# Performance work log

Measured on AMD Instinct MI355X. Metric: run time of the kernel, lower is better.

## Reference

```python
import jax, jax.numpy as jnp
import numpy as np

B, N, K = 8, 1024, 16        # graphs, points per graph, kNN fan-in (loop=True includes self)
LATENT = 256
EPS = 1e-5                   # PyG BatchNorm eps


def _bn(x, g, b):
    # training-mode batch norm over all leading (node/edge) dims, per channel
    ax = tuple(range(x.ndim - 1))
    mu = jnp.mean(x, axis=ax, keepdims=True)
    var = jnp.var(x, axis=ax, keepdims=True)
    return g * (x - mu) * jax.lax.rsqrt(var + EPS) + b


def setup_inputs() -> dict:
    key = jax.random.key(0)
    ks = jax.random.split(key, 12)

    def lin(k, fi, fo):
        s = (6.0 / (fi + fo)) ** 0.5
        kw, kb = jax.random.split(k)
        W = jax.random.uniform(kw, (fi, fo), jnp.float32, -s, s)
        bb = jax.random.uniform(kb, (fo,), jnp.float32, -s, s)
        return W, bb

    pos = jax.random.normal(ks[0], (B * N, 3), jnp.float32)
    batch = jnp.repeat(jnp.arange(B, dtype=jnp.int32), N)

    c1_W1, c1_b1 = lin(ks[1], 6, 64)
    c1_W2, c1_b2 = lin(ks[2], 64, 64)
    c2_W1, c2_b1 = lin(ks[3], 67, 64)
    c2_W2, c2_b2 = lin(ks[4], 64, 128)
    c2_W3, c2_b3 = lin(ks[5], 128, 1024)
    lin_W, lin_b = lin(ks[6], 1024, LATENT)

    return {
        "pos": pos, "batch": batch,
        "c1_W1": c1_W1, "c1_b1": c1_b1,
        "c1_g1": jnp.ones((64,), jnp.float32), "c1_be1": jnp.zeros((64,), jnp.float32),
        "c1_W2": c1_W2, "c1_b2": c1_b2,
        "c2_W1": c2_W1, "c2_b1": c2_b1,
        "c2_g1": jnp.ones((64,), jnp.float32), "c2_be1": jnp.zeros((64,), jnp.float32),
        "c2_W2": c2_W2, "c2_b2": c2_b2,
        "c2_g2": jnp.ones((128,), jnp.float32), "c2_be2": jnp.zeros((128,), jnp.float32),
        "c2_W3": c2_W3, "c2_b3": c2_b3,
        "lin_W": lin_W, "lin_b": lin_b,
        "lin_g": jnp.ones((LATENT,), jnp.float32), "lin_be": jnp.zeros((LATENT,), jnp.float32),
    }


def reference(pos, batch,
              c1_W1, c1_b1, c1_g1, c1_be1, c1_W2, c1_b2,
              c2_W1, c2_b1, c2_g1, c2_be1, c2_W2, c2_b2,
              c2_g2, c2_be2, c2_W3, c2_b3,
              lin_W, lin_b, lin_g, lin_be):
    # ---- kNN graph (per-graph, loop=True: self is nearest) ----
    p3 = pos.reshape(B, N, 3)
    sq = jnp.sum(p3 * p3, axis=-1)                                   # [B,N]
    d = sq[:, :, None] + sq[:, None, :] - 2.0 * jnp.einsum('bnd,bmd->bnm', p3, p3)
    _, nbr = jax.lax.top_k(-d, K)                                    # [B,N,K] neighbor ids
    idx = (nbr + (jnp.arange(B) * N)[:, None, None]).reshape(B * N, K)

    # ---- PointNetConv 1: gather -> MLP([6,64,64]) -> max aggregate ----
    pj = pos[idx]                                                    # [P,K,3]
    rel = pj - pos[:, None, :]                                       # [P,K,3]
    feat = jnp.concatenate([pj, rel], axis=-1)                       # [P,K,6]
    h = jax.nn.relu(_bn(feat @ c1_W1 + c1_b1, c1_g1, c1_be1))
    x1 = jnp.max(h @ c1_W2 + c1_b2, axis=1)                          # [P,64]

    # ---- PointNetConv 2: MLP([67,64,128,1024]) -> max aggregate ----
    feat2 = jnp.concatenate([x1[idx], rel], axis=-1)                 # [P,K,67]
    h = jax.nn.relu(_bn(feat2 @ c2_W1 + c2_b1, c2_g1, c2_be1))
    h = jax.nn.relu(_bn(h @ c2_W2 + c2_b2, c2_g2, c2_be2))
    x2 = jnp.max(h @ c2_W3 + c2_b3, axis=1)                          # [P,1024]

    # ---- global max pool per graph + final MLP (plain_last=False) ----
    g = x2.reshape(B, N, -1).max(axis=1)                             # [B,1024]
    return jax.nn.relu(_bn(g @ lin_W + lin_b, lin_g, lin_be))        # [B,LATENT]
```

## Files before the change

kernel.cpp:

```cpp
#include <hip/hip_runtime.h>
#include <hip/hip_cooperative_groups.h>
#include <math.h>

#define NB   8
#define NPTS 1024
#define PTS  8192
#define KNN  16
#define PK   (PTS*KNN)

typedef __attribute__((ext_vector_type(8))) _Float16 f16x8;
typedef __attribute__((ext_vector_type(4))) float f32x4;

__device__ __forceinline__ unsigned short f2h(float f) {
  _Float16 h = (_Float16)f;
  union { _Float16 h; unsigned short u; } c; c.h = h;
  return c.u;
}
__device__ __forceinline__ float h2f(unsigned short u) {
  union { unsigned short u; _Float16 h; } c; c.u = u;
  return (float)c.h;
}
__device__ __forceinline__ int lanerank(unsigned long long m) {
  return __builtin_amdgcn_mbcnt_hi((unsigned)(m >> 32),
         __builtin_amdgcn_mbcnt_lo((unsigned)m, 0));
}

__global__ __launch_bounds__(256) void knn_conv1_kernel(const float* __restrict__ pos,
    const float* __restrict__ W1, const float* __restrict__ b1,
    int* __restrict__ idx, float* __restrict__ rel,
    unsigned short* __restrict__ z1h, float* __restrict__ mid1) {
  __shared__ float px[NPTS], py[NPTS], pz[NPTS];
  __shared__ float feat[4][KNN][6];
  __shared__ float ls[256], ls2[256];
  const int t = threadIdx.x;
  const int wv = t >> 6, lane = t & 63;
  const int b = blockIdx.x;
  const int graph = b >> 8;
  const int base = graph << 10;
  for (int j = t; j < NPTS; j += 256) {
    px[j] = pos[3*(base+j)];
    py[j] = pos[3*(base+j)+1];
    pz[j] = pos[3*(base+j)+2];
  }
  __syncthreads();

  const int il = ((b & 255) << 2) + wv;
  const int i  = base + il;
  const float pix = px[il], piy = py[il], piz = pz[il];
  const float sqi = pix*pix + piy*piy + piz*piz;

  unsigned key[16];
  #pragma unroll
  for (int q = 0; q < 16; ++q) {
    const int j = (q << 6) + lane;
    const float x = px[j], y = py[j], z = pz[j];
    const float sqj = x*x + y*y + z*z;
    const float dt  = pix*x + piy*y + piz*z;
    const float d   = sqi + sqj - 2.0f*dt;
    const unsigned db = __float_as_uint(d);
    key[q] = (db >> 31) ? ~db : (db | 0x80000000u);
  }

  unsigned V = 0;
  #pragma unroll 1
  for (int bb = 31; bb >= 0; --bb) {
    const unsigned test = V | (1u << bb);
    int cnt = 0;
    #pragma unroll
    for (int q = 0; q < 16; ++q)
      cnt += __popcll(__ballot(key[q] < test));
    if (cnt < 16) V = test;
  }

  int c = 0;
  #pragma unroll
  for (int q = 0; q < 16; ++q)
    c += __popcll(__ballot(key[q] < V));

  int p_lt = 0, p_eq = c;
  #pragma unroll 1
  for (int q = 0; q < 16; ++q) {
    const unsigned long long mlt = __ballot(key[q] < V);
    const unsigned long long meq = __ballot(key[q] == V);
    int slot = -1;
    if (key[q] < V) slot = p_lt + lanerank(mlt);
    else if (key[q] == V) {
      const int s = p_eq + lanerank(meq);
      if (s < 16) slot = s;
    }
    if (slot >= 0) {
      const int j = (q << 6) + lane;
      const int r = i*KNN + slot;
      const float rx = px[j] - pix, ry = py[j] - piy, rz = pz[j] - piz;
      idx[r] = base + j;
      rel[3*r] = rx; rel[3*r+1] = ry; rel[3*r+2] = rz;
      feat[wv][slot][0] = px[j]; feat[wv][slot][1] = py[j]; feat[wv][slot][2] = pz[j];
      feat[wv][slot][3] = rx;    feat[wv][slot][4] = ry;    feat[wv][slot][5] = rz;
    }
    p_lt += __popcll(mlt);
    p_eq += __popcll(meq);
  }

  float w[6];
  #pragma unroll
  for (int q = 0; q < 6; ++q) w[q] = W1[q*64 + lane];
  const float bbv = b1[lane];
  float s = 0.0f, s2 = 0.0f;
  #pragma unroll
  for (int k = 0; k < KNN; ++k) {
    float z = bbv;
    #pragma unroll
    for (int q = 0; q < 6; ++q) z += feat[wv][k][q]*w[q];
    z1h[(size_t)(i*KNN + k)*64 + lane] = f2h(z);
    s += z; s2 += z*z;
  }
  ls[t] = s; ls2[t] = s2;
  __syncthreads();
  if (t < 64) {
    float a  = ls[t] + ls[t+64] + ls[t+128] + ls[t+192];
    float a2 = ls2[t] + ls2[t+64] + ls2[t+128] + ls2[t+192];
    const int cp = (b & 7) * 128;
    atomicAdd(&mid1[cp + t], a);
    atomicAdd(&mid1[cp + 64 + t], a2);
  }
}

__global__ __launch_bounds__(256) void wprep_kernel(const float* __restrict__ W3,
    const float* __restrict__ W2, const float* __restrict__ W1c2,
    const float* __restrict__ W2c1,
    unsigned short* __restrict__ W3T, unsigned short* __restrict__ W2T,
    unsigned short* __restrict__ w1T, unsigned short* __restrict__ W2c1T,
    float* __restrict__ mids) {
  const int b = blockIdx.x, t = threadIdx.x;
  if (b < 128) {
    const int k = b;
    const int ks = k >> 5, qd = (k >> 3) & 3, e = k & 7;
    for (int n = t; n < 1024; n += 256) {
      const int nb = n >> 4, mc = n & 15;
      W3T[((nb*4 + ks) << 9) + qd*128 + mc*8 + e] = f2h(W3[(size_t)k*1024 + n]);
    }
  } else if (b < 132) {
    for (int id = (b-128)*2048 + t; id < (b-127)*2048; id += 256) {
      const int n = id >> 6, k = id & 63;
      W2T[n*64 + k] = f2h(W2[k*128 + n]);
    }
  } else if (b < 136) {
    for (int id = (b-132)*1024 + t; id < (b-131)*1024; id += 256) {
      const int n = id >> 6, k = id & 63;
      w1T[n*64 + k] = f2h(W1c2[k*64 + n]);
    }
  } else if (b < 140) {
    for (int id = (b-136)*1024 + t; id < (b-135)*1024; id += 256) {
      const int n = id >> 6, k = id & 63;
      W2c1T[n*64 + k] = f2h(W2c1[k*64 + n]);
    }
  } else {
    for (int i2 = t; i2 < 4096; i2 += 256) mids[i2] = 0.0f;
  }
}

__global__ __launch_bounds__(256) void conv1_l2max_mfma(
    const unsigned short* __restrict__ z1h, const float* __restrict__ mid1,
    const float* __restrict__ g1, const float* __restrict__ be1,
    const unsigned short* __restrict__ W2T, const float* __restrict__ b2,
    unsigned short* __restrict__ x1h) {
  __shared__ unsigned short As[128*64];
  __shared__ float scl[64], shl[64];
  const int r0 = blockIdx.x * 128;
  const int t = threadIdx.x;
  const int lane = t & 63, w = t >> 6;
  const int quad = lane >> 4, mcol = lane & 15;
  const float invR = 1.0f / (float)PK;

  if (t < 64) {
    float s = 0.0f, s2 = 0.0f;
    #pragma unroll
    for (int k = 0; k < 8; ++k) { s += mid1[k*128 + t]; s2 += mid1[k*128 + 64 + t]; }
    const float mu  = s * invR;
    const float var = s2 * invR - mu*mu;
    const float sc  = g1[t] * rsqrtf(var + 1e-5f);
    scl[t] = sc; shl[t] = be1[t] - mu*sc;
  }
  __syncthreads();

  {
    const int kb = t & 7, rr = t >> 3;
    float sc[8], sh[8];
    #pragma unroll
    for (int q = 0; q < 8; ++q) { sc[q] = scl[kb*8 + q]; sh[q] = shl[kb*8 + q]; }
    #pragma unroll
    for (int it = 0; it < 4; ++it) {
      const int r = rr + it*32;
      union { uint4 v; unsigned short s[8]; } in;
      in.v = *(const uint4*)(z1h + (size_t)(r0 + r)*64 + kb*8);
      union { unsigned short s[8]; uint4 v; } o;
      #pragma unroll
      for (int q = 0; q < 8; ++q)
        o.s[q] = f2h(fmaxf(h2f(in.s[q])*sc[q] + sh[q], 0.0f));
      *(uint4*)(As + r*64 + ((kb ^ (r & 7)) * 8)) = o.v;
    }
  }
  __syncthreads();

  const int wrow = (w >> 1) * 64;
  const int wncol = (w & 1) * 32;

  f32x4 acc[4][2];
  #pragma unroll
  for (int mi = 0; mi < 4; ++mi)
    #pragma unroll
    for (int ni = 0; ni < 2; ++ni)
      acc[mi][ni] = (f32x4){0.f, 0.f, 0.f, 0.f};

  #pragma unroll
  for (int ks = 0; ks < 2; ++ks) {
    f16x8 af[4], bfr[2];
    #pragma unroll
    for (int mi = 0; mi < 4; ++mi) {
      const int row = wrow + mi*16 + mcol;
      af[mi] = *(const f16x8*)(As + row*64 + (((ks*4 + quad) ^ (row & 7)) * 8));
    }
    #pragma unroll
    for (int ni = 0; ni < 2; ++ni) {
      const int nr = wncol + ni*16 + mcol;
      bfr[ni] = *(const f16x8*)(W2T + nr*64 + ks*32 + quad*8);
    }
    #pragma unroll
    for (int mi = 0; mi < 4; ++mi)
      #pragma unroll
      for (int ni = 0; ni < 2; ++ni)
        acc[mi][ni] = __builtin_amdgcn_mfma_f32_16x16x32_f16(af[mi], bfr[ni], acc[mi][ni], 0, 0, 0);
  }

  float bb[2];
  #pragma unroll
  for (int ni = 0; ni < 2; ++ni) bb[ni] = b2[wncol + ni*16 + mcol];
  #pragma unroll
  for (int mi = 0; mi < 4; ++mi) {
    const int p = blockIdx.x*8 + (w >> 1)*4 + mi;
    #pragma unroll
    for (int ni = 0; ni < 2; ++ni) {
      f32x4 a = acc[mi][ni];
      float m = fmaxf(fmaxf(a[0], a[1]), fmaxf(a[2], a[3]));
      m = fmaxf(m, __shfl_xor(m, 16));
      m = fmaxf(m, __shfl_xor(m, 32));
      if (quad == 0) x1h[(size_t)p*64 + wncol + ni*16 + mcol] = f2h(m + bb[ni]);
    }
  }
}

__global__ __launch_bounds__(256) void conv2_l1_mfma(
    const unsigned short* __restrict__ x1h, const int* __restrict__ idx,
    const float* __restrict__ rel, const unsigned short* __restrict__ w1T,
    const float* __restrict__ W1full, const float* __restrict__ b1,
    unsigned short* __restrict__ zah, float* __restrict__ midA) {
  __shared__ unsigned short S[128*64];
  __shared__ int   idxr[128];
  __shared__ float rl[128*3];
  __shared__ float ps[256];
  const int r0 = blockIdx.x * 128;
  const int t = threadIdx.x;
  const int lane = t & 63, w = t >> 6;
  const int quad = lane >> 4, mcol = lane & 15;

  if (t < 128) idxr[t] = idx[r0 + t];
  else if (t < 224) *(float4*)(rl + (t-128)*4) = *(const float4*)(rel + (size_t)r0*3 + (t-128)*4);
  __syncthreads();

  {
    const int kb = t & 7, rr = t >> 3;
    #pragma unroll
    for (int it = 0; it < 4; ++it) {
      const int r = rr + it*32;
      const int gj = idxr[r];
      const uint4 v = *(const uint4*)(x1h + (size_t)gj*64 + kb*8);
      *(uint4*)(S + r*64 + ((kb ^ (r & 7)) * 8)) = v;
    }
  }
  __syncthreads();

  const int wrow = (w >> 1) * 64;
  const int wcol = (w & 1) * 32;

  f16x8 af[2][4], bfr[2][2];
  #pragma unroll
  for (int ks = 0; ks < 2; ++ks)
    #pragma unroll
    for (int mi = 0; mi < 4; ++mi) {
      const int row = wrow + mi*16 + mcol;
      af[ks][mi] = *(const f16x8*)(S + row*64 + (((ks*4 + quad) ^ (row & 7)) * 8));
    }
  #pragma unroll
  for (int ks = 0; ks < 2; ++ks)
    #pragma unroll
    for (int ni = 0; ni < 2; ++ni) {
      const int nr = wcol + ni*16 + mcol;
      bfr[ks][ni] = *(const f16x8*)(w1T + nr*64 + ks*32 + quad*8);
    }

  f32x4 acc[4][2];
  #pragma unroll
  for (int mi = 0; mi < 4; ++mi)
    #pragma unroll
    for (int ni = 0; ni < 2; ++ni)
      acc[mi][ni] = (f32x4){0.f, 0.f, 0.f, 0.f};

  #pragma unroll
  for (int ks = 0; ks < 2; ++ks)
    #pragma unroll
    for (int mi = 0; mi < 4; ++mi)
      #pragma unroll
      for (int ni = 0; ni < 2; ++ni)
        acc[mi][ni] = __builtin_amdgcn_mfma_f32_16x16x32_f16(af[ks][mi], bfr[ks][ni], acc[mi][ni], 0, 0, 0);

  __syncthreads();

  float bb[2], wr0[2], wr1[2], wr2[2];
  #pragma unroll
  for (int ni = 0; ni < 2; ++ni) {
    const int col = wcol + ni*16 + mcol;
    bb[ni]  = b1[col];
    wr0[ni] = W1full[64*64 + col];
    wr1[ni] = W1full[65*64 + col];
    wr2[ni] = W1full[66*64 + col];
  }
  float s[2] = {0,0}, s2[2] = {0,0};
  #pragma unroll
  for (int mi = 0; mi < 4; ++mi) {
    #pragma unroll
    for (int j = 0; j < 4; ++j) {
      const int row = wrow + mi*16 + quad*4 + j;
      const float r0v = rl[row*3], r1v = rl[row*3+1], r2v = rl[row*3+2];
      #pragma unroll
      for (int ni = 0; ni < 2; ++ni) {
        const int col = wcol + ni*16 + mcol;
        const int g = col >> 3, o = col & 7;
        const float v = acc[mi][ni][j] + bb[ni] + r0v*wr0[ni] + r1v*wr1[ni] + r2v*wr2[ni];
        S[row*64 + ((g ^ (row & 7)) << 3) + o] = f2h(v);
        s[ni] += v; s2[ni] += v*v;
      }
    }
  }
  #pragma unroll
  for (int ni = 0; ni < 2; ++ni) {
    s[ni]  += __shfl_xor(s[ni], 16);  s[ni]  += __shfl_xor(s[ni], 32);
    s2[ni] += __shfl_xor(s2[ni], 16); s2[ni] += __shfl_xor(s2[ni], 32);
  }
  if (quad == 0) {
    const int rh = w >> 1;
    #pragma unroll
    for (int ni = 0; ni < 2; ++ni) {
      const int col = wcol + ni*16 + mcol;
      ps[rh*128 + col]      = s[ni];
      ps[rh*128 + 64 + col] = s2[ni];
    }
  }
  __syncthreads();

  #pragma unroll
  for (int i = 0; i < 4; ++i) {
    const int u = i*256 + t;
    const int row = u >> 3, gg = u & 7;
    *(uint4*)(zah + (size_t)(r0 + row)*64 + gg*8) =
        *(const uint4*)(S + row*64 + ((gg ^ (row & 7)) << 3));
  }
  if (t < 128) atomicAdd(&midA[(blockIdx.x & 7)*128 + t], ps[t] + ps[128 + t]);
}

__global__ __launch_bounds__(256) void conv2_l2_mfma(
    const unsigned short* __restrict__ zah, const float* __restrict__ midA,
    const float* __restrict__ g1, const float* __restrict__ be1,
    const unsigned short* __restrict__ W2T, const float* __restrict__ b2,
    unsigned short* __restrict__ zhb, float* __restrict__ midB) {
  __shared__ unsigned short S[128*128];
  __shared__ float ps[512];
  __shared__ float scl[64], shl[64];
  const int r0 = blockIdx.x * 128;
  const int t = threadIdx.x;
  const int lane = t & 63, w = t >> 6;
  const int quad = lane >> 4, mcol = lane & 15;
  const float invR = 1.0f / (float)PK;

  if (t < 64) {
    float s = 0.0f, s2 = 0.0f;
    #pragma unroll
    for (int k = 0; k < 8; ++k) { s += midA[k*128 + t]; s2 += midA[k*128 + 64 + t]; }
    const float mu  = s * invR;
    const float var = s2 * invR - mu*mu;
    const float sc  = g1[t] * rsqrtf(var + 1e-5f);
    scl[t] = sc; shl[t] = be1[t] - mu*sc;
  }
  __syncthreads();

  {
    const int kb = t & 7, rr = t >> 3;
    float sc[8], sh[8];
    #pragma unroll
    for (int q = 0; q < 8; ++q) { sc[q] = scl[kb*8 + q]; sh[q] = shl[kb*8 + q]; }
    #pragma unroll
    for (int it = 0; it < 4; ++it) {
      const int r = rr + it*32;
      union { uint4 v; unsigned short s[8]; } in;
      in.v = *(const uint4*)(zah + (size_t)(r0 + r)*64 + kb*8);
      union { unsigned short s[8]; uint4 v; } o;
      #pragma unroll
      for (int q = 0; q < 8; ++q)
        o.s[q] = f2h(fmaxf(h2f(in.s[q])*sc[q] + sh[q], 0.0f));
      *(uint4*)(S + r*64 + ((kb ^ (r & 7)) * 8)) = o.v;
    }
  }
  __syncthreads();

  const int wrow = (w >> 1) * 64;
  const int wcol = (w & 1) * 64;

  f16x8 af[2][4], bfr[2][4];
  #pragma unroll
  for (int ks = 0; ks < 2; ++ks)
    #pragma unroll
    for (int mi = 0; mi < 4; ++mi) {
      const int row = wrow + mi*16 + mcol;
      af[ks][mi] = *(const f16x8*)(S + row*64 + (((ks*4 + quad) ^ (row & 7)) * 8));
    }
  #pragma unroll
  for (int ks = 0; ks < 2; ++ks)
    #pragma unroll
    for (int ni = 0; ni < 4; ++ni) {
      const int nr = wcol + ni*16 + mcol;
      bfr[ks][ni] = *(const f16x8*)(W2T + nr*64 + ks*32 + quad*8);
    }

  f32x4 acc[4][4];
  #pragma unroll
  for (int mi = 0; mi < 4; ++mi)
    #pragma unroll
    for (int ni = 0; ni < 4; ++ni)
      acc[mi][ni] = (f32x4){0.f, 0.f, 0.f, 0.f};

  #pragma unroll
  for (int ks = 0; ks < 2; ++ks)
    #pragma unroll
    for (int mi = 0; mi < 4; ++mi)
      #pragma unroll
      for (int ni = 0; ni < 4; ++ni)
        acc[mi][ni] = __builtin_amdgcn_mfma_f32_16x16x32_f16(af[ks][mi], bfr[ks][ni], acc[mi][ni], 0, 0, 0);

  __syncthreads();

  float bb[4];
  #pragma unroll
  for (int ni = 0; ni < 4; ++ni) bb[ni] = b2[wcol + ni*16 + mcol];
  float s[4] = {0,0,0,0}, s2[4] = {0,0,0,0};
  #pragma unroll
  for (int mi = 0; mi < 4; ++mi) {
    #pragma unroll
    for (int ni = 0; ni < 4; ++ni) {
      const int col = wcol + ni*16 + mcol;
      const int g = col >> 3, o = col & 7;
      #pragma unroll
      for (int j = 0; j < 4; ++j) {
        const int row = wrow + mi*16 + quad*4 + j;
        const float v = acc[mi][ni][j] + bb[ni];
        S[row*128 + ((g ^ (row & 15)) << 3) + o] = f2h(v);
        s[ni] += v; s2[ni] += v*v;
      }
    }
  }
  #pragma unroll
  for (int ni = 0; ni < 4; ++ni) {
    s[ni]  += __shfl_xor(s[ni], 16);  s[ni]  += __shfl_xor(s[ni], 32);
    s2[ni] += __shfl_xor(s2[ni], 16); s2[ni] += __shfl_xor(s2[ni], 32);
  }
  if (quad == 0) {
    const int rh = w >> 1;
    #pragma unroll
    for (int ni = 0; ni < 4; ++ni) {
      const int col = wcol + ni*16 + mcol;
      ps[rh*256 + col]       = s[ni];
      ps[rh*256 + 128 + col] = s2[ni];
    }
  }
  __syncthreads();

  #pragma unroll
  for (int i = 0; i < 8; ++i) {
    const int u = i*256 + t;
    const int row = u >> 4, gg = u & 15;
    *(uint4*)(zhb + (size_t)(r0 + row)*128 + gg*8) =
        *(const uint4*)(S + row*128 + ((gg ^ (row & 15)) << 3));
  }
  atomicAdd(&midB[(blockIdx.x & 7)*256 + t], ps[t] + ps[256 + t]);
}

__global__ __launch_bounds__(256, 3) void conv2_l3max_mfma(
    const unsigned short* __restrict__ zhb, const float* __restrict__ midB,
    const float* __restrict__ g2, const float* __restrict__ be2,
    const unsigned short* __restrict__ W3T,
    float* __restrict__ pmax2) {
  __shared__ unsigned short As[128*128];
  __shared__ float pm[2048];
  float* const scl = pm;
  float* const shl = pm + 128;
  const int rb = blockIdx.x;
  const int r0 = rb * 128;
  const int t = threadIdx.x;
  const int lane = t & 63, w = t >> 6;
  const int quad = lane >> 4, mcol = lane & 15;
  const float invR = 1.0f / (float)PK;

  if (t < 128) {
    float s = 0.0f, s2 = 0.0f;
    #pragma unroll
    for (int k = 0; k < 8; ++k) { s += midB[k*256 + t]; s2 += midB[k*256 + 128 + t]; }
    const float mu  = s * invR;
    const float var = s2 * invR - mu*mu;
    const float sc  = g2[t] * rsqrtf(var + 1e-5f);
    scl[t] = sc; shl[t] = be2[t] - mu*sc;
  }
  __syncthreads();

  {
    const int kb = t & 15, rr = t >> 4;
    float sc[8], sh[8];
    #pragma unroll
    for (int q = 0; q < 8; ++q) { sc[q] = scl[kb*8 + q]; sh[q] = shl[kb*8 + q]; }
    #pragma unroll
    for (int it = 0; it < 8; ++it) {
      const int r = rr + it*16;
      union { uint4 v; unsigned short s[8]; } in;
      in.v = *(const uint4*)(zhb + (size_t)(r0 + r)*128 + kb*8);
      union { unsigned short s[8]; uint4 v; } o;
      #pragma unroll
      for (int q = 0; q < 8; ++q)
        o.s[q] = f2h(fmaxf(h2f(in.s[q])*sc[q] + sh[q], 0.0f));
      *(uint4*)(As + r*128 + ((kb ^ (r & 7)) * 8)) = o.v;
    }
  }
  __syncthreads();

  const int wrow = (w >> 1) * 64;
  const int wncol = (w & 1) * 32;
  const int rh = w >> 1;

  #pragma unroll 1
  for (int chunk = 0; chunk < 16; ++chunk) {
    const int nb0 = chunk*4 + (w & 1)*2;

    f32x4 acc[4][2];
    #pragma unroll
    for (int mi = 0; mi < 4; ++mi)
      #pragma unroll
      for (int ni = 0; ni < 2; ++ni)
        acc[mi][ni] = (f32x4){0.f, 0.f, 0.f, 0.f};

    #pragma unroll
    for (int ks = 0; ks < 4; ++ks) {
      f16x8 bfr[2], af[4];
      #pragma unroll
      for (int ni = 0; ni < 2; ++ni)
        bfr[ni] = *(const f16x8*)(W3T + (((nb0 + ni)*4 + ks) << 9) + lane*8);
      #pragma unroll
      for (int mi = 0; mi < 4; ++mi) {
        const int row = wrow + mi*16 + mcol;
        af[mi] = *(const f16x8*)(As + row*128 + (((ks*4 + quad) ^ (row & 7)) * 8));
      }
      #pragma unroll
      for (int mi = 0; mi < 4; ++mi)
        #pragma unroll
        for (int ni = 0; ni < 2; ++ni)
          acc[mi][ni] = __builtin_amdgcn_mfma_f32_16x16x32_f16(af[mi], bfr[ni], acc[mi][ni], 0, 0, 0);
    }

    #pragma unroll
    for (int ni = 0; ni < 2; ++ni) {
      float m4 = -INFINITY;
      #pragma unroll
      for (int mi = 0; mi < 4; ++mi) {
        f32x4 a = acc[mi][ni];
        m4 = fmaxf(m4, fmaxf(fmaxf(a[0], a[1]), fmaxf(a[2], a[3])));
      }
      m4 = fmaxf(m4, __shfl_xor(m4, 16));
      m4 = fmaxf(m4, __shfl_xor(m4, 32));
      if (quad == 0)
        pm[rh*1024 + chunk*64 + wncol + ni*16 + mcol] = m4;
    }
  }
  __syncthreads();

  #pragma unroll
  for (int i = 0; i < 4; ++i) {
    const int c = i*256 + t;
    pmax2[(size_t)rb*1024 + c] = fmaxf(pm[c], pm[1024 + c]);
  }
}

__global__ __launch_bounds__(256, 2) void conv2_fused2(
    const unsigned short* __restrict__ x1h, const int* __restrict__ idx,
    const float* __restrict__ rel, const unsigned short* __restrict__ w1T,
    const float* __restrict__ W1full, const float* __restrict__ b1,
    float* __restrict__ midA,
    const unsigned short* __restrict__ W2T, const float* __restrict__ b2,
    float* __restrict__ midB,
    const float* __restrict__ g1, const float* __restrict__ be1,
    const float* __restrict__ g2, const float* __restrict__ be2,
    const unsigned short* __restrict__ W3T,
    float* __restrict__ pmax2) {
  cooperative_groups::grid_group grid = cooperative_groups::this_grid();
  __shared__ unsigned short As2[32768];
  __shared__ float pscratch[1024];
  const int t = threadIdx.x;
  const int lane = t & 63, w = t >> 6;
  const int quad = lane >> 4, mcol = lane & 15;
  const int rh = w >> 1;
  const int wrow = rh * 64;
  const float invR = 1.0f / (float)PK;

  #pragma unroll 1
  for (int tp = 0; tp < 2; ++tp) {
    const int rb = blockIdx.x + tp*512;
    const int r0 = rb * 128;
    const int vb = tp ? 24576 : 0;
    int*   idxr = (int*)pscratch;
    float* rl   = pscratch + 128;
    float* ps   = pscratch + 512;
    if (t < 128) idxr[t] = idx[r0 + t];
    else if (t < 224) *(float4*)(rl + (t-128)*4) = *(const float4*)(rel + (size_t)r0*3 + (t-128)*4);
    __syncthreads();

    {
      const int kb = t & 7, rr = t >> 3;
      #pragma unroll
      for (int it = 0; it < 4; ++it) {
        const int r = rr + it*32;
        const int gj = idxr[r];
        const uint4 v = *(const uint4*)(x1h + (size_t)gj*64 + kb*8);
        *(uint4*)(As2 + 8192 + r*64 + ((kb ^ (r & 7)) * 8)) = v;
      }
    }
    __syncthreads();

    const int wcol = (w & 1) * 32;
    f16x8 af[2][4], bfr[2][2];
    #pragma unroll
    for (int ks = 0; ks < 2; ++ks)
      #pragma unroll
      for (int mi = 0; mi < 4; ++mi) {
        const int row = wrow + mi*16 + mcol;
        af[ks][mi] = *(const f16x8*)(As2 + 8192 + row*64 + (((ks*4 + quad) ^ (row & 7)) * 8));
      }
    #pragma unroll
    for (int ks = 0; ks < 2; ++ks)
      #pragma unroll
      for (int ni = 0; ni < 2; ++ni) {
        const int nr = wcol + ni*16 + mcol;
        bfr[ks][ni] = *(const f16x8*)(w1T + nr*64 + ks*32 + quad*8);
      }

    f32x4 acc[4][2];
    #pragma unroll
    for (int mi = 0; mi < 4; ++mi)
      #pragma unroll
      for (int ni = 0; ni < 2; ++ni)
        acc[mi][ni] = (f32x4){0.f, 0.f, 0.f, 0.f};
    #pragma unroll
    for (int ks = 0; ks < 2; ++ks)
      #pragma unroll
      for (int mi = 0; mi < 4; ++mi)
        #pragma unroll
        for (int ni = 0; ni < 2; ++ni)
          acc[mi][ni] = __builtin_amdgcn_mfma_f32_16x16x32_f16(af[ks][mi], bfr[ks][ni], acc[mi][ni], 0, 0, 0);

    float bb[2], wr0[2], wr1[2], wr2[2];
    #pragma unroll
    for (int ni = 0; ni < 2; ++ni) {
      const int col = wcol + ni*16 + mcol;
      bb[ni]  = b1[col];
      wr0[ni] = W1full[64*64 + col];
      wr1[ni] = W1full[65*64 + col];
      wr2[ni] = W1full[66*64 + col];
    }
    float s[2] = {0,0}, s2[2] = {0,0};
    #pragma unroll
    for (int mi = 0; mi < 4; ++mi) {
      #pragma unroll
      for (int j = 0; j < 4; ++j) {
        const int row = wrow + mi*16 + quad*4 + j;
        const float r0v = rl[row*3], r1v = rl[row*3+1], r2v = rl[row*3+2];
        #pragma unroll
        for (int ni = 0; ni < 2; ++ni) {
          const int col = wcol + ni*16 + mcol;
          const int g = col >> 3, o = col & 7;
          const float v = acc[mi][ni][j] + bb[ni] + r0v*wr0[ni] + r1v*wr1[ni] + r2v*wr2[ni];
          As2[vb + row*64 + ((g ^ (row & 7)) << 3) + o] = f2h(v);
          s[ni] += v; s2[ni] += v*v;
        }
      }
    }
    #pragma unroll
    for (int ni = 0; ni < 2; ++ni) {
      s[ni]  += __shfl_xor(s[ni], 16);  s[ni]  += __shfl_xor(s[ni], 32);
      s2[ni] += __shfl_xor(s2[ni], 16); s2[ni] += __shfl_xor(s2[ni], 32);
    }
    if (quad == 0) {
      #pragma unroll
      for (int ni = 0; ni < 2; ++ni) {
        const int col = wcol + ni*16 + mcol;
        ps[rh*128 + col]      = s[ni];
        ps[rh*128 + 64 + col] = s2[ni];
      }
    }
    __syncthreads();
    if (t < 128) atomicAdd(&midA[(rb & 7)*128 + t], ps[t] + ps[128 + t]);
  }

  grid.sync();

  {
    float* scl = pscratch;
    float* shl = pscratch + 64;
    float* ps2 = pscratch + 512;
    if (t < 64) {
      float s = 0.0f, s2 = 0.0f;
      #pragma unroll
      for (int k = 0; k < 8; ++k) { s += midA[k*128 + t]; s2 += midA[k*128 + 64 + t]; }
      const float mu  = s * invR;
      const float var = s2 * invR - mu*mu;
      const float sc  = g1[t] * rsqrtf(var + 1e-5f);
      scl[t] = sc; shl[t] = be1[t] - mu*sc;
    }
    __syncthreads();
    {
      const int kb = t & 7, rr = t >> 3;
      float sc[8], sh[8];
      #pragma unroll
      for (int q = 0; q < 8; ++q) { sc[q] = scl[kb*8 + q]; sh[q] = shl[kb*8 + q]; }
      #pragma unroll
      for (int tb = 0; tb < 2; ++tb) {
        const int vb = tb ? 24576 : 0;
        #pragma unroll
        for (int it = 0; it < 4; ++it) {
          const int r = rr + it*32;
          unsigned short* a = As2 + vb + r*64 + ((kb ^ (r & 7)) * 8);
          union { uint4 v; unsigned short s[8]; } in; in.v = *(const uint4*)a;
          union { unsigned short s[8]; uint4 v; } o;
          #pragma unroll
          for (int q = 0; q < 8; ++q)
            o.s[q] = f2h(fmaxf(h2f(in.s[q])*sc[q] + sh[q], 0.0f));
          *(uint4*)a = o.v;
        }
      }
    }
    __syncthreads();

    #pragma unroll 1
    for (int tp = 0; tp < 2; ++tp) {
      const int rb = blockIdx.x + tp*512;
      const int vb = tp ? 24576 : 0;
      const int zb = tp * 16384;
      f16x8 af[2][4];
      #pragma unroll
      for (int ks = 0; ks < 2; ++ks)
        #pragma unroll
        for (int mi = 0; mi < 4; ++mi) {
          const int row = wrow + mi*16 + mcol;
          af[ks][mi] = *(const f16x8*)(As2 + vb + row*64 + (((ks*4 + quad) ^ (row & 7)) * 8));
        }
      __syncthreads();

      #pragma unroll
      for (int half = 0; half < 2; ++half) {
        const int wcol = (w & 1)*64 + half*32;
        f16x8 bfr[2][2];
        #pragma unroll
        for (int ks = 0; ks < 2; ++ks)
          #pragma unroll
          for (int ni = 0; ni < 2; ++ni) {
            const int nr = wcol + ni*16 + mcol;
            bfr[ks][ni] = *(const f16x8*)(W2T + nr*64 + ks*32 + quad*8);
          }
        f32x4 acc[4][2];
        #pragma unroll
        for (int mi = 0; mi < 4; ++mi)
          #pragma unroll
          for (int ni = 0; ni < 2; ++ni)
            acc[mi][ni] = (f32x4){0.f, 0.f, 0.f, 0.f};
        #pragma unroll
        for (int ks = 0; ks < 2; ++ks)
          #pragma unroll
          for (int mi = 0; mi < 4; ++mi)
            #pragma unroll
            for (int ni = 0; ni < 2; ++ni)
              acc[mi][ni] = __builtin_amdgcn_mfma_f32_16x16x32_f16(af[ks][mi], bfr[ks][ni], acc[mi][ni], 0, 0, 0);

        float bb[2];
        #pragma unroll
        for (int ni = 0; ni < 2; ++ni) bb[ni] = b2[wcol + ni*16 + mcol];
        float s[2] = {0,0}, s2[2] = {0,0};
        #pragma unroll
        for (int mi = 0; mi < 4; ++mi) {
          #pragma unroll
          for (int ni = 0; ni < 2; ++ni) {
            const int col = wcol + ni*16 + mcol;
            const int g = col >> 3, o = col & 7;
            #pragma unroll
            for (int j = 0; j < 4; ++j) {
              const int row = wrow + mi*16 + quad*4 + j;
              const float v = acc[mi][ni][j] + bb[ni];
              As2[zb + row*128 + ((g ^ (row & 7)) << 3) + o] = f2h(v);
              s[ni] += v; s2[ni] += v*v;
            }
          }
        }
        #pragma unroll
        for (int ni = 0; ni < 2; ++ni) {
          s[ni]  += __shfl_xor(s[ni], 16);  s[ni]  += __shfl_xor(s[ni], 32);
          s2[ni] += __shfl_xor(s2[ni], 16); s2[ni] += __shfl_xor(s2[ni], 32);
        }
        if (quad == 0) {
          #pragma unroll
          for (int ni = 0; ni < 2; ++ni) {
            const int col = wcol + ni*16 + mcol;
            ps2[rh*256 + col]       = s[ni];
            ps2[rh*256 + 128 + col] = s2[ni];
          }
        }
      }
      __syncthreads();
      atomicAdd(&midB[(rb & 7)*256 + t], ps2[t] + ps2[t + 256]);
    }
  }

  grid.sync();

  {
    float* scl = pscratch;
    float* shl = pscratch + 128;
    if (t < 128) {
      float s = 0.0f, s2 = 0.0f;
      #pragma unroll
      for (int k = 0; k < 8; ++k) { s += midB[k*256 + t]; s2 += midB[k*256 + 128 + t]; }
      const float mu  = s * invR;
      const float var = s2 * invR - mu*mu;
      const float sc  = g2[t] * rsqrtf(var + 1e-5f);
      scl[t] = sc; shl[t] = be2[t] - mu*sc;
    }
    __syncthreads();
    {
      const int kb = t & 15, rr = t >> 4;
      float sc[8], sh[8];
      #pragma unroll
      for (int q = 0; q < 8; ++q) { sc[q] = scl[kb*8 + q]; sh[q] = shl[kb*8 + q]; }
      #pragma unroll
      for (int tb = 0; tb < 2; ++tb) {
        const int zb = tb * 16384;
        #pragma unroll
        for (int it = 0; it < 8; ++it) {
          const int r = rr + it*16;
          unsigned short* a = As2 + zb + r*128 + ((kb ^ (r & 7)) * 8);
          union { uint4 v; unsigned short s[8]; } in; in.v = *(const uint4*)a;
          union { unsigned short s[8]; uint4 v; } o;
          #pragma unroll
          for (int q = 0; q < 8; ++q)
            o.s[q] = f2h(fmaxf(h2f(in.s[q])*sc[q] + sh[q], 0.0f));
          *(uint4*)a = o.v;
        }
      }
    }
    __syncthreads();

    const int wncol = (w & 1) * 32;
    #pragma unroll 1
    for (int tp = 0; tp < 2; ++tp) {
      const int rb = blockIdx.x + tp*512;
      const int zb = tp * 16384;
      #pragma unroll 1
      for (int chunk = 0; chunk < 16; ++chunk) {
        const int nb0 = chunk*4 + (w & 1)*2;
        f32x4 acc[4][2];
        #pragma unroll
        for (int mi = 0; mi < 4; ++mi)
          #pragma unroll
          for (int ni = 0; ni < 2; ++ni)
            acc[mi][ni] = (f32x4){0.f, 0.f, 0.f, 0.f};

        #pragma unroll
        for (int ks = 0; ks < 4; ++ks) {
          f16x8 bfr[2], af[4];
          #pragma unroll
          for (int ni = 0; ni < 2; ++ni)
            bfr[ni] = *(const f16x8*)(W3T + (((nb0 + ni)*4 + ks) << 9) + lane*8);
          #pragma unroll
          for (int mi = 0; mi < 4; ++mi) {
            const int row = wrow + mi*16 + mcol;
            af[mi] = *(const f16x8*)(As2 + zb + row*128 + (((ks*4 + quad) ^ (row & 7)) * 8));
          }
          #pragma unroll
          for (int mi = 0; mi < 4; ++mi)
            #pragma unroll
            for (int ni = 0; ni < 2; ++ni)
              acc[mi][ni] = __builtin_amdgcn_mfma_f32_16x16x32_f16(af[mi], bfr[ni], acc[mi][ni], 0, 0, 0);
        }

        #pragma unroll
        for (int ni = 0; ni < 2; ++ni) {
          float m4 = -INFINITY;
          #pragma unroll
          for (int mi = 0; mi < 4; ++mi) {
            f32x4 a = acc[mi][ni];
            m4 = fmaxf(m4, fmaxf(fmaxf(a[0], a[1]), fmaxf(a[2], a[3])));
          }
          m4 = fmaxf(m4, __shfl_xor(m4, 16));
          m4 = fmaxf(m4, __shfl_xor(m4, 32));
          if (quad == 0)
            pmax2[((size_t)rh << 20) + (size_t)rb*1024 + chunk*64 + wncol + ni*16 + mcol] = m4;
        }
      }
    }
  }
}

__global__ __launch_bounds__(256) void poollin_kernel(const float* __restrict__ pmax2,
    const float* __restrict__ b3, const float* __restrict__ W,
    float* __restrict__ zpart, int two_plane) {
  __shared__ float gs[256];
  const int b = blockIdx.x >> 2, q = blockIdx.x & 3;
  const int t = threadIdx.x;
  const int c = q*256 + t;
  const float* p0 = pmax2 + (size_t)b*128*1024 + c;
  float m = -INFINITY;
  if (two_plane) {
    const float* p1 = p0 + (1u << 20);
    #pragma unroll 4
    for (int rb = 0; rb < 128; ++rb)
      m = fmaxf(m, fmaxf(p0[(size_t)rb*1024], p1[(size_t)rb*1024]));
  } else {
    #pragma unroll 4
    for (int rb = 0; rb < 128; ++rb) m = fmaxf(m, p0[(size_t)rb*1024]);
  }
  gs[t] = m + b3[c];
  __syncthreads();
  const float* Wq = W + (size_t)q*256*256;
  float acc = 0.0f;
  for (int cc = 0; cc < 256; ++cc) acc += gs[cc] * Wq[cc*256 + t];
  zpart[blockIdx.x*256 + t] = acc;
}

__global__ __launch_bounds__(256) void final_kernel(const float* __restrict__ zpart,
    const float* __restrict__ lb, const float* __restrict__ lg,
    const float* __restrict__ lbe, float* __restrict__ out) {
  const int o = threadIdx.x;
  float z[NB]; float s = 0.0f, s2 = 0.0f;
  #pragma unroll
  for (int b = 0; b < NB; ++b) {
    float v = lb[o];
    #pragma unroll
    for (int q = 0; q < 4; ++q) v += zpart[(b*4+q)*256 + o];
    z[b] = v; s += v; s2 += v*v;
  }
  const float mu  = s * 0.125f;
  const float var = s2 * 0.125f - mu*mu;
  const float inv = rsqrtf(var + 1e-5f);
  const float sc = lg[o]*inv, sh = lbe[o] - mu*sc;
  #pragma unroll
  for (int b = 0; b < NB; ++b) out[b*256 + o] = fmaxf(z[b]*sc + sh, 0.0f);
}

extern "C" void kernel_launch(void* const* d_in, const int* in_sizes, int n_in,
                              void* d_out, int out_size, void* d_ws, size_t ws_size,
                              hipStream_t stream) {
  const float* pos    = (const float*)d_in[0];
  const float* c1_W1  = (const float*)d_in[2];
  const float* c1_b1  = (const float*)d_in[3];
  const float* c1_g1  = (const float*)d_in[4];
  const float* c1_be1 = (const float*)d_in[5];
  const float* c1_W2  = (const float*)d_in[6];
  const float* c1_b2  = (const float*)d_in[7];
  const float* c2_W1  = (const float*)d_in[8];
  const float* c2_b1  = (const float*)d_in[9];
  const float* c2_g1  = (const float*)d_in[10];
  const float* c2_be1 = (const float*)d_in[11];
  const float* c2_W2  = (const float*)d_in[12];
  const float* c2_b2  = (const float*)d_in[13];
  const float* c2_g2  = (const float*)d_in[14];
  const float* c2_be2 = (const float*)d_in[15];
  const float* c2_W3  = (const float*)d_in[16];
  const float* c2_b3  = (const float*)d_in[17];
  const float* lin_W  = (const float*)d_in[18];
  const float* lin_b  = (const float*)d_in[19];
  const float* lin_g  = (const float*)d_in[20];
  const float* lin_be = (const float*)d_in[21];
  float* out = (float*)d_out;

  char* ws = (char*)d_ws;
  int*   idx     = (int*)  (ws + 0);
  float* rel     = (float*)(ws + 524288);
  float* zpart   = (float*)(ws + 2097152 + 2048);
  float* mid1    = (float*)(ws + 2164736);
  float* midA    = (float*)(ws + 2164736 + 4096);
  float* midB    = (float*)(ws + 2164736 + 8192);
  unsigned short* W2T   = (unsigned short*)(ws + 2295808);
  unsigned short* w1T   = (unsigned short*)(ws + 2312192);
  unsigned short* W2c1T = (unsigned short*)(ws + 2320384);
  unsigned short* z1h = (unsigned short*)(ws + 2426880);
  unsigned short* zah = (unsigned short*)(ws + 2426880);
  float* pmax2   = (float*)(ws + 2426880);
  unsigned short* x1h = (unsigned short*)(ws + 35981312);
  unsigned short* zhb = (unsigned short*)(ws + 38078464);
  unsigned short* W3T = (unsigned short*)(ws + 71632896);

  wprep_kernel<<<141, 256, 0, stream>>>(c2_W3, c2_W2, c2_W1, c1_W2, W3T, W2T, w1T, W2c1T, mid1);
  knn_conv1_kernel<<<PTS/4, 256, 0, stream>>>(pos, c1_W1, c1_b1, idx, rel, z1h, mid1);
  conv1_l2max_mfma<<<PK/128, 256, 0, stream>>>(z1h, mid1, c1_g1, c1_be1, W2c1T, c1_b2, x1h);

  int nb = 0;
  hipError_t qe = hipOccupancyMaxActiveBlocksPerMultiprocessor(
      &nb, (const void*)conv2_fused2, 256, 0);
  hipError_t ce = hipErrorUnknown;
  if (qe == hipSuccess && nb >= 2) {
    void* cargs[] = {
      (void*)&x1h, (void*)&idx, (void*)&rel, (void*)&w1T, (void*)&c2_W1, (void*)&c2_b1,
      (void*)&midA, (void*)&W2T, (void*)&c2_b2, (void*)&midB,
      (void*)&c2_g1, (void*)&c2_be1, (void*)&c2_g2, (void*)&c2_be2,
      (void*)&W3T, (void*)&pmax2
    };
    ce = hipLaunchCooperativeKernel((const void*)conv2_fused2, dim3(512), dim3(256),
                                    cargs, 0, stream);
  }
  const int coop_ok = (ce == hipSuccess) ? 1 : 0;
  if (!coop_ok) {
    conv2_l1_mfma<<<PK/128, 256, 0, stream>>>(x1h, idx, rel, w1T, c2_W1, c2_b1, zah, midA);
    conv2_l2_mfma<<<PK/128, 256, 0, stream>>>(zah, midA, c2_g1, c2_be1, W2T, c2_b2, zhb, midB);
    conv2_l3max_mfma<<<PK/128, 256, 0, stream>>>(zhb, midB, c2_g2, c2_be2, W3T, pmax2);
  }

  poollin_kernel<<<NB*4, 256, 0, stream>>>(pmax2, c2_b3, lin_W, zpart, coop_ok);
  final_kernel<<<1, 256, 0, stream>>>(zpart, lin_b, lin_g, lin_be, out);
}
```

Baseline: 228.1 us.

## Process both row tiles concurrently in a 512-thread cooperative conv2 block

The fused cooperative conv2 kernel now launches 512 threads per block instead of 256. Each 256-thread half handles one of the two 128-row tiles that were previously processed one after the other in a loop, using separate LDS staging and scratch regions. The aim is to double the waves resident per CU and overlap the two tiles' gathers, MFMA work and batch-norm passes instead of serialising them. In exchange the block is larger and the launch bounds cap registers per thread, which could cause spills. The cooperative launch also depends on two such blocks fitting per CU in LDS.

New measurement: 228.8 us. About the same (+0.3%).

```diff
diff --git a/kernel.cpp b/kernel.cpp
--- a/kernel.cpp
+++ b/kernel.cpp
@@ -594,7 +594,7 @@
   }
 }
 
-__global__ __launch_bounds__(256, 2) void conv2_fused2(
+__global__ __launch_bounds__(512, 4) void conv2_fused3(
     const unsigned short* __restrict__ x1h, const int* __restrict__ idx,
     const float* __restrict__ rel, const unsigned short* __restrict__ w1T,
     const float* __restrict__ W1full, const float* __restrict__ b1,
@@ -607,46 +607,51 @@
     float* __restrict__ pmax2) {
   cooperative_groups::grid_group grid = cooperative_groups::this_grid();
   __shared__ unsigned short As2[32768];
-  __shared__ float pscratch[1024];
+  __shared__ float pscratch[2048];
   const int t = threadIdx.x;
-  const int lane = t & 63, w = t >> 6;
+  const int tl = t & 255;
+  const int tp = t >> 8;
+  const int lane = t & 63;
+  const int wl = (t >> 6) & 3;
   const int quad = lane >> 4, mcol = lane & 15;
-  const int rh = w >> 1;
+  const int rh = wl >> 1;
   const int wrow = rh * 64;
+  const int rb = blockIdx.x + tp*512;
+  const int r0 = rb * 128;
+  const int vOff  = tp ? 24576 : 0;
+  const int stOff = 8192 + tp*8192;
+  const int zOff  = tp * 16384;
+  float* const scratch = pscratch + tp*1024;
   const float invR = 1.0f / (float)PK;
 
-  #pragma unroll 1
-  for (int tp = 0; tp < 2; ++tp) {
-    const int rb = blockIdx.x + tp*512;
-    const int r0 = rb * 128;
-    const int vb = tp ? 24576 : 0;
-    int*   idxr = (int*)pscratch;
-    float* rl   = pscratch + 128;
-    float* ps   = pscratch + 512;
-    if (t < 128) idxr[t] = idx[r0 + t];
-    else if (t < 224) *(float4*)(rl + (t-128)*4) = *(const float4*)(rel + (size_t)r0*3 + (t-128)*4);
+  {
+    int*   idxr = (int*)scratch;
+    float* rl   = scratch + 128;
+    float* ps   = scratch + 512;
+    if (tl < 128) idxr[tl] = idx[r0 + tl];
+    else if (tl < 224) *(float4*)(rl + (tl-128)*4) = *(const float4*)(rel + (size_t)r0*3 + (tl-128)*4);
     __syncthreads();
 
     {
-      const int kb = t & 7, rr = t >> 3;
+      const int kb = tl & 7, rr = tl >> 3;
       #pragma unroll
       for (int it = 0; it < 4; ++it) {
         const int r = rr + it*32;
         const int gj = idxr[r];
         const uint4 v = *(const uint4*)(x1h + (size_t)gj*64 + kb*8);
-        *(uint4*)(As2 + 8192 + r*64 + ((kb ^ (r & 7)) * 8)) = v;
+        *(uint4*)(As2 + stOff + r*64 + ((kb ^ (r & 7)) * 8)) = v;
       }
     }
     __syncthreads();
 
-    const int wcol = (w & 1) * 32;
+    const int wcol = (wl & 1) * 32;
     f16x8 af[2][4], bfr[2][2];
     #pragma unroll
     for (int ks = 0; ks < 2; ++ks)
       #pragma unroll
       for (int mi = 0; mi < 4; ++mi) {
         const int row = wrow + mi*16 + mcol;
-        af[ks][mi] = *(const f16x8*)(As2 + 8192 + row*64 + (((ks*4 + quad) ^ (row & 7)) * 8));
+        af[ks][mi] = *(const f16x8*)(As2 + stOff + row*64 + (((ks*4 + quad) ^ (row & 7)) * 8));
       }
     #pragma unroll
     for (int ks = 0; ks < 2; ++ks)
@@ -691,7 +696,7 @@
           const int col = wcol + ni*16 + mcol;
           const int g = col >> 3, o = col & 7;
           const float v = acc[mi][ni][j] + bb[ni] + r0v*wr0[ni] + r1v*wr1[ni] + r2v*wr2[ni];
-          As2[vb + row*64 + ((g ^ (row & 7)) << 3) + o] = f2h(v);
+          As2[vOff + row*64 + ((g ^ (row & 7)) << 3) + o] = f2h(v);
           s[ni] += v; s2[ni] += v*v;
         }
       }
@@ -710,7 +715,7 @@
       }
     }
     __syncthreads();
-    if (t < 128) atomicAdd(&midA[(rb & 7)*128 + t], ps[t] + ps[128 + t]);
+    if (tl < 128) atomicAdd(&midA[(rb & 7)*128 + tl], ps[tl] + ps[128 + tl]);
   }
 
   grid.sync();
@@ -718,7 +723,7 @@
   {
     float* scl = pscratch;
     float* shl = pscratch + 64;
-    float* ps2 = pscratch + 512;
+    float* ps2 = pscratch + 512 + tp*512;
     if (t < 64) {
       float s = 0.0f, s2 = 0.0f;
       #pragma unroll
@@ -730,104 +735,94 @@
     }
     __syncthreads();
     {
-      const int kb = t & 7, rr = t >> 3;
+      const int kb = tl & 7, rr = tl >> 3;
       float sc[8], sh[8];
       #pragma unroll
       for (int q = 0; q < 8; ++q) { sc[q] = scl[kb*8 + q]; sh[q] = shl[kb*8 + q]; }
       #pragma unroll
-      for (int tb = 0; tb < 2; ++tb) {
-        const int vb = tb ? 24576 : 0;
-        #pragma unroll
-        for (int it = 0; it < 4; ++it) {
-          const int r = rr + it*32;
-          unsigned short* a = As2 + vb + r*64 + ((kb ^ (r & 7)) * 8);
-          union { uint4 v; unsigned short s[8]; } in; in.v = *(const uint4*)a;
-          union { unsigned short s[8]; uint4 v; } o;
-          #pragma unroll
-          for (int q = 0; q < 8; ++q)
-            o.s[q] = f2h(fmaxf(h2f(in.s[q])*sc[q] + sh[q], 0.0f));
-          *(uint4*)a = o.v;
+      for (int it = 0; it < 4; ++it) {
+        const int r = rr + it*32;
+        unsigned short* a = As2 + vOff + r*64 + ((kb ^ (r & 7)) * 8);
+        union { uint4 v; unsigned short s[8]; } in; in.v = *(const uint4*)a;
+        union { unsigned short s[8]; uint4 v; } o;
+        #pragma unroll
+        for (int q = 0; q < 8; ++q)
+          o.s[q] = f2h(fmaxf(h2f(in.s[q])*sc[q] + sh[q], 0.0f));
+        *(uint4*)a = o.v;
+      }
+    }
+    __syncthreads();
+
+    f16x8 af[2][4];
+    #pragma unroll
+    for (int ks = 0; ks < 2; ++ks)
+      #pragma unroll
+      for (int mi = 0; mi < 4; ++mi) {
+        const int row = wrow + mi*16 + mcol;
+        af[ks][mi] = *(const f16x8*)(As2 + vOff + row*64 + (((ks*4 + quad) ^ (row & 7)) * 8));
+      }
+    __syncthreads();
+
+    #pragma unroll
+    for (int half = 0; half < 2; ++half) {
+      const int wcol = (wl & 1)*64 + half*32;
+      f16x8 bfr[2][2];
+      #pragma unroll
+      for (int ks = 0; ks < 2; ++ks)
+        #pragma unroll
+        for (int ni = 0; ni < 2; ++ni) {
+          const int nr = wcol + ni*16 + mcol;
+          bfr[ks][ni] = *(const f16x8*)(W2T + nr*64 + ks*32 + quad*8);
         }
-      }
-    }
-    __syncthreads();
-
-    #pragma unroll 1
-    for (int tp = 0; tp < 2; ++tp) {
-      const int rb = blockIdx.x + tp*512;
-      const int vb = tp ? 24576 : 0;
-      const int zb = tp * 16384;
-      f16x8 af[2][4];
+      f32x4 acc[4][2];
+      #pragma unroll
+      for (int mi = 0; mi < 4; ++mi)
+        #pragma unroll
+        for (int ni = 0; ni < 2; ++ni)
+          acc[mi][ni] = (f32x4){0.f, 0.f, 0.f, 0.f};
       #pragma unroll
       for (int ks = 0; ks < 2; ++ks)
-        #pragma unroll
-        for (int mi = 0; mi < 4; ++mi) {
-          const int row = wrow + mi*16 + mcol;
-          af[ks][mi] = *(const f16x8*)(As2 + vb + row*64 + (((ks*4 + quad) ^ (row & 7)) * 8));
-        }
-      __syncthreads();
-
-      #pragma unroll
-      for (int half = 0; half < 2; ++half) {
-        const int wcol = (w & 1)*64 + half*32;
-        f16x8 bfr[2][2];
-        #pragma unroll
-        for (int ks = 0; ks < 2; ++ks)
-          #pragma unroll
-          for (int ni = 0; ni < 2; ++ni) {
-            const int nr = wcol + ni*16 + mcol;
-            bfr[ks][ni] = *(const f16x8*)(W2T + nr*64 + ks*32 + quad*8);
-          }
-        f32x4 acc[4][2];
         #pragma unroll
         for (int mi = 0; mi < 4; ++mi)
           #pragma unroll
           for (int ni = 0; ni < 2; ++ni)
-            acc[mi][ni] = (f32x4){0.f, 0.f, 0.f, 0.f};
-        #pragma unroll
-        for (int ks = 0; ks < 2; ++ks)
+            acc[mi][ni] = __builtin_amdgcn_mfma_f32_16x16x32_f16(af[ks][mi], bfr[ks][ni], acc[mi][ni], 0, 0, 0);
+
+      float bb[2];
+      #pragma unroll
+      for (int ni = 0; ni < 2; ++ni) bb[ni] = b2[wcol + ni*16 + mcol];
+      float s[2] = {0,0}, s2[2] = {0,0};
+      #pragma unroll
+      for (int mi = 0; mi < 4; ++mi) {
+        #pragma unroll
+        for (int ni = 0; ni < 2; ++ni) {
+          const int col = wcol + ni*16 + mcol;
+          const int g = col >> 3, o = col & 7;
           #pragma unroll
-          for (int mi = 0; mi < 4; ++mi)
-            #pragma unroll
-            for (int ni = 0; ni < 2; ++ni)
-              acc[mi][ni] = __builtin_amdgcn_mfma_f32_16x16x32_f16(af[ks][mi], bfr[ks][ni], acc[mi][ni], 0, 0, 0);
-
-        float bb[2];
-        #pragma unroll
-        for (int ni = 0; ni < 2; ++ni) bb[ni] = b2[wcol + ni*16 + mcol];
-        float s[2] = {0,0}, s2[2] = {0,0};
-        #pragma unroll
-        for (int mi = 0; mi < 4; ++mi) {
-          #pragma unroll
-          for (int ni = 0; ni < 2; ++ni) {
-            const int col = wcol + ni*16 + mcol;
-            const int g = col >> 3, o = col & 7;
-            #pragma unroll
-            for (int j = 0; j < 4; ++j) {
-              const int row = wrow + mi*16 + quad*4 + j;
-              const float v = acc[mi][ni][j] + bb[ni];
-              As2[zb + row*128 + ((g ^ (row & 7)) << 3) + o] = f2h(v);
-              s[ni] += v; s2[ni] += v*v;
-            }
+          for (int j = 0; j < 4; ++j) {
+            const int row = wrow + mi*16 + quad*4 + j;
+            const float v = acc[mi][ni][j] + bb[ni];
+            As2[zOff + row*128 + ((g ^ (row & 7)) << 3) + o] = f2h(v);
+            s[ni] += v; s2[ni] += v*v;
           }
         }
+      }
+      #pragma unroll
+      for (int ni = 0; ni < 2; ++ni) {
+        s[ni]  += __shfl_xor(s[ni], 16);  s[ni]  += __shfl_xor(s[ni], 32);
+        s2[ni] += __shfl_xor(s2[ni], 16); s2[ni] += __shfl_xor(s2[ni], 32);
+      }
+      if (quad == 0) {
         #pragma unroll
         for (int ni = 0; ni < 2; ++ni) {
-          s[ni]  += __shfl_xor(s[ni], 16);  s[ni]  += __shfl_xor(s[ni], 32);
-          s2[ni] += __shfl_xor(s2[ni], 16); s2[ni] += __shfl_xor(s2[ni], 32);
+          const int col = wcol + ni*16 + mcol;
+          ps2[rh*256 + col]       = s[ni];
+          ps2[rh*256 + 128 + col] = s2[ni];
         }
-        if (quad == 0) {
-          #pragma unroll
-          for (int ni = 0; ni < 2; ++ni) {
-            const int col = wcol + ni*16 + mcol;
-            ps2[rh*256 + col]       = s[ni];
-            ps2[rh*256 + 128 + col] = s2[ni];
-          }
-        }
-      }
-      __syncthreads();
-      atomicAdd(&midB[(rb & 7)*256 + t], ps2[t] + ps2[t + 256]);
-    }
+      }
+    }
+    __syncthreads();
+    atomicAdd(&midB[(rb & 7)*256 + tl], ps2[tl] + ps2[tl + 256]);
   }
 
   grid.sync();
@@ -846,74 +841,65 @@
     }
     __syncthreads();
     {
-      const int kb = t & 15, rr = t >> 4;
+      const int kb = tl & 15, rr = tl >> 4;
       float sc[8], sh[8];
       #pragma unroll
       for (int q = 0; q < 8; ++q) { sc[q] = scl[kb*8 + q]; sh[q] = shl[kb*8 + q]; }
       #pragma unroll
-      for (int tb = 0; tb < 2; ++tb) {
-        const int zb = tb * 16384;
-        #pragma unroll
-        for (int it = 0; it < 8; ++it) {
-          const int r = rr + it*16;
-          unsigned short* a = As2 + zb + r*128 + ((kb ^ (r & 7)) * 8);
-          union { uint4 v; unsigned short s[8]; } in; in.v = *(const uint4*)a;
-          union { unsigned short s[8]; uint4 v; } o;
-          #pragma unroll
-          for (int q = 0; q < 8; ++q)
-            o.s[q] = f2h(fmaxf(h2f(in.s[q])*sc[q] + sh[q], 0.0f));
-          *(uint4*)a = o.v;
+      for (int it = 0; it < 8; ++it) {
+        const int r = rr + it*16;
+        unsigned short* a = As2 + zOff + r*128 + ((kb ^ (r & 7)) * 8);
+        union { uint4 v; unsigned short s[8]; } in; in.v = *(const uint4*)a;
+        union { unsigned short s[8]; uint4 v; } o;
+        #pragma unroll
+        for (int q = 0; q < 8; ++q)
+          o.s[q] = f2h(fmaxf(h2f(in.s[q])*sc[q] + sh[q], 0.0f));
+        *(uint4*)a = o.v;
+      }
+    }
+    __syncthreads();
+
+    const int wncol = (wl & 1) * 32;
+    #pragma unroll 1
+    for (int chunk = 0; chunk < 16; ++chunk) {
+      const int nb0 = chunk*4 + (wl & 1)*2;
+      f32x4 acc[4][2];
+      #pragma unroll
+      for (int mi = 0; mi < 4; ++mi)
+        #pragma unroll
+        for (int ni = 0; ni < 2; ++ni)
+          acc[mi][ni] = (f32x4){0.f, 0.f, 0.f, 0.f};
+
+      #pragma unroll
+      for (int ks = 0; ks < 4; ++ks) {
+        f16x8 bfr[2], af[4];
+        #pragma unroll
+        for (int ni = 0; ni < 2; ++ni)
+          bfr[ni] = *(const f16x8*)(W3T + (((nb0 + ni)*4 + ks) << 9) + lane*8);
+        #pragma unroll
+        for (int mi = 0; mi < 4; ++mi) {
+          const int row = wrow + mi*16 + mcol;
+          af[mi] = *(const f16x8*)(As2 + zOff + row*128 + (((ks*4 + quad) ^ (row & 7)) * 8));
         }
-      }
-    }
-    __syncthreads();
-
-    const int wncol = (w & 1) * 32;
-    #pragma unroll 1
-    for (int tp = 0; tp < 2; ++tp) {
-      const int rb = blockIdx.x + tp*512;
-      const int zb = tp * 16384;
-      #pragma unroll 1
-      for (int chunk = 0; chunk < 16; ++chunk) {
-        const int nb0 = chunk*4 + (w & 1)*2;
-        f32x4 acc[4][2];
         #pragma unroll
         for (int mi = 0; mi < 4; ++mi)
           #pragma unroll
           for (int ni = 0; ni < 2; ++ni)
-            acc[mi][ni] = (f32x4){0.f, 0.f, 0.f, 0.f};
-
-        #pragma unroll
-        for (int ks = 0; ks < 4; ++ks) {
-          f16x8 bfr[2], af[4];
-          #pragma unroll
-          for (int ni = 0; ni < 2; ++ni)
-            bfr[ni] = *(const f16x8*)(W3T + (((nb0 + ni)*4 + ks) << 9) + lane*8);
-          #pragma unroll
-          for (int mi = 0; mi < 4; ++mi) {
-            const int row = wrow + mi*16 + mcol;
-            af[mi] = *(const f16x8*)(As2 + zb + row*128 + (((ks*4 + quad) ^ (row & 7)) * 8));
-          }
-          #pragma unroll
-          for (int mi = 0; mi < 4; ++mi)
-            #pragma unroll
-            for (int ni = 0; ni < 2; ++ni)
-              acc[mi][ni] = __builtin_amdgcn_mfma_f32_16x16x32_f16(af[mi], bfr[ni], acc[mi][ni], 0, 0, 0);
+            acc[mi][ni] = __builtin_amdgcn_mfma_f32_16x16x32_f16(af[mi], bfr[ni], acc[mi][ni], 0, 0, 0);
+      }
+
+      #pragma unroll
+      for (int ni = 0; ni < 2; ++ni) {
+        float m4 = -INFINITY;
+        #pragma unroll
+        for (int mi = 0; mi < 4; ++mi) {
+          f32x4 a = acc[mi][ni];
+          m4 = fmaxf(m4, fmaxf(fmaxf(a[0], a[1]), fmaxf(a[2], a[3])));
         }
-
-        #pragma unroll
-        for (int ni = 0; ni < 2; ++ni) {
-          float m4 = -INFINITY;
-          #pragma unroll
-          for (int mi = 0; mi < 4; ++mi) {
-            f32x4 a = acc[mi][ni];
-            m4 = fmaxf(m4, fmaxf(fmaxf(a[0], a[1]), fmaxf(a[2], a[3])));
-          }
-          m4 = fmaxf(m4, __shfl_xor(m4, 16));
-          m4 = fmaxf(m4, __shfl_xor(m4, 32));
-          if (quad == 0)
-            pmax2[((size_t)rh << 20) + (size_t)rb*1024 + chunk*64 + wncol + ni*16 + mcol] = m4;
-        }
+        m4 = fmaxf(m4, __shfl_xor(m4, 16));
+        m4 = fmaxf(m4, __shfl_xor(m4, 32));
+        if (quad == 0)
+          pmax2[((size_t)rh << 20) + (size_t)rb*1024 + chunk*64 + wncol + ni*16 + mcol] = m4;
       }
     }
   }
@@ -1014,7 +1000,7 @@
 
   int nb = 0;
   hipError_t qe = hipOccupancyMaxActiveBlocksPerMultiprocessor(
-      &nb, (const void*)conv2_fused2, 256, 0);
+      &nb, (const void*)conv2_fused3, 512, 0);
   hipError_t ce = hipErrorUnknown;
   if (qe == hipSuccess && nb >= 2) {
     void* cargs[] = {
@@ -1023,7 +1009,7 @@
       (void*)&c2_g1, (void*)&c2_be1, (void*)&c2_g2, (void*)&c2_be2,
       (void*)&W3T, (void*)&pmax2
     };
-    ce = hipLaunchCooperativeKernel((const void*)conv2_fused2, dim3(512), dim3(256),
+    ce = hipLaunchCooperativeKernel((const void*)conv2_fused3, dim3(512), dim3(512),
                                     cargs, 0, stream);
   }
   const int coop_ok = (ce == hipSuccess) ? 1 : 0;
```
